# Optimization experiments

Measured on AMD Instinct MI355X. Metric: run time of the kernel, lower is better.

The kernel has to match this reference:

```python
import jax, jax.numpy as jnp
import numpy as np

B, H, S, D = 16, 12, 1024, 64  # batch, heads, seq, head_dim (dim=768, num_head=12)


def setup_inputs() -> dict:
    key = jax.random.key(0)
    ks = jax.random.split(key, 9)
    sc = 1.0 / np.sqrt(D)
    return {
        "x": jax.random.normal(ks[0], (B, H, S, D), dtype=jnp.float32),
        "Wq": jax.random.normal(ks[1], (D, D), dtype=jnp.float32) * sc,
        "bq": jax.random.normal(ks[2], (D,), dtype=jnp.float32) * 0.02,
        "Wk": jax.random.normal(ks[3], (D, D), dtype=jnp.float32) * sc,
        "bk": jax.random.normal(ks[4], (D,), dtype=jnp.float32) * 0.02,
        "Wv": jax.random.normal(ks[5], (D, D), dtype=jnp.float32) * sc,
        "bv": jax.random.normal(ks[6], (D,), dtype=jnp.float32) * 0.02,
        "Wo": jax.random.normal(ks[7], (D, D), dtype=jnp.float32) * sc,
        "bo": jax.random.normal(ks[8], (D,), dtype=jnp.float32) * 0.02,
    }


def reference(x, Wq, bq, Wk, bk, Wv, bv, Wo, bo):
    # torch Linear: y = x @ W^T + b, applied to last dim (head_dim)
    q = jnp.einsum("bhsd,ed->bhse", x, Wq) + bq
    k = jnp.einsum("bhsd,ed->bhse", x, Wk) + bk
    v = jnp.einsum("bhsd,ed->bhse", x, Wv) + bv
    scores = jnp.einsum("bhqd,bhkd->bhqk", q, k) / jnp.sqrt(jnp.float32(q.shape[-1]))
    attn = jax.nn.softmax(scores, axis=-1)
    out = jnp.einsum("bhqk,bhkd->bhqd", attn, v)
    out = jnp.einsum("bhsd,ed->bhse", out, Wo) + bo
    return out
```

## Files before the change

kernel.cpp:

```cpp
#include <hip/hip_runtime.h>
#include <math.h>


typedef __bf16 bf16x8 __attribute__((ext_vector_type(8)));
typedef float  f32x4  __attribute__((ext_vector_type(4)));

#define MFMA(a, b, c) __builtin_amdgcn_mfma_f32_16x16x32_bf16((a), (b), (c), 0, 0, 0)

static constexpr int S = 1024;
static constexpr int LDS_PAD = 72;
static constexpr size_t NE = 196608ull * 64ull;
static constexpr float QSCALE = 0.125f * 1.4426950408889634f;

__device__ inline unsigned long long pack4bf(float a, float b, float c, float d) {
    union { __bf16 h[4]; unsigned long long u; } pk;
    pk.h[0] = (__bf16)a; pk.h[1] = (__bf16)b; pk.h[2] = (__bf16)c; pk.h[3] = (__bf16)d;
    return pk.u;
}

__global__ __launch_bounds__(256) void proj_qkv(
    const float* __restrict__ x,
    const float* __restrict__ Wq, const float* __restrict__ bq,
    const float* __restrict__ Wk, const float* __restrict__ bk,
    const float* __restrict__ Wv, const float* __restrict__ bv,
    __bf16* __restrict__ gq, __bf16* __restrict__ gk, __bf16* __restrict__ gvt)
{
    __shared__ __align__(16) __bf16 lx[128][LDS_PAD];
    __shared__ __align__(16) __bf16 lw[3][64][LDS_PAD];
    __shared__ float lb[3][64];

    const int tid = threadIdx.x;
    const int row_base = blockIdx.x * 128;

    #pragma unroll
    for (int i = tid * 4; i < 8192; i += 1024) {
        float4 v = *(const float4*)(x + (size_t)row_base * 64 + i);
        int r = i >> 6, c = i & 63;
        *(unsigned long long*)&lx[r][c] = pack4bf(v.x, v.y, v.z, v.w);
    }
    const float* Ws[3] = {Wq, Wk, Wv};
    #pragma unroll
    for (int mtx = 0; mtx < 3; mtx++) {
        #pragma unroll
        for (int i = tid * 4; i < 4096; i += 1024) {
            float4 v = *(const float4*)(Ws[mtx] + i);
            int r = i >> 6, c = i & 63;
            *(unsigned long long*)&lw[mtx][r][c] = pack4bf(v.x, v.y, v.z, v.w);
        }
    }
    if (tid < 64) { lb[0][tid] = bq[tid]; lb[1][tid] = bk[tid]; lb[2][tid] = bv[tid]; }
    __syncthreads();

    const int w = tid >> 6, lane = tid & 63, m = lane & 15, quad = lane >> 4;
    const int bh = row_base >> 10;
    const int s_base = row_base & 1023;

    bf16x8 xf[2][2];
    #pragma unroll
    for (int g = 0; g < 2; g++) {
        xf[g][0] = *(const bf16x8*)&lx[w * 32 + g * 16 + m][quad * 8];
        xf[g][1] = *(const bf16x8*)&lx[w * 32 + g * 16 + m][32 + quad * 8];
    }

    #pragma unroll
    for (int mtx = 0; mtx < 3; mtx++) {
        #pragma unroll
        for (int et = 0; et < 4; et++) {
            bf16x8 wf0 = *(const bf16x8*)&lw[mtx][et * 16 + m][quad * 8];
            bf16x8 wf1 = *(const bf16x8*)&lw[mtx][et * 16 + m][32 + quad * 8];
            if (mtx < 2) {
                float4 bias = *(const float4*)&lb[mtx][et * 16 + quad * 4];
                #pragma unroll
                for (int g = 0; g < 2; g++) {
                    f32x4 acc = {0.f, 0.f, 0.f, 0.f};
                    acc = MFMA(wf0, xf[g][0], acc);
                    acc = MFMA(wf1, xf[g][1], acc);
                    size_t row = (size_t)row_base + w * 32 + g * 16 + m;
                    unsigned long long u;
                    if (mtx == 0)
                        u = pack4bf((acc[0] + bias.x) * QSCALE, (acc[1] + bias.y) * QSCALE,
                                    (acc[2] + bias.z) * QSCALE, (acc[3] + bias.w) * QSCALE);
                    else
                        u = pack4bf(acc[0] + bias.x, acc[1] + bias.y,
                                    acc[2] + bias.z, acc[3] + bias.w);
                    __bf16* dst = (mtx == 0 ? gq : gk);
                    *(unsigned long long*)(dst + row * 64 + et * 16 + quad * 4) = u;
                }
            } else {
                const int e = et * 16 + m;
                const float bias = lb[2][e];
                #pragma unroll
                for (int g = 0; g < 2; g++) {
                    f32x4 acc = {0.f, 0.f, 0.f, 0.f};
                    acc = MFMA(xf[g][0], wf0, acc);
                    acc = MFMA(xf[g][1], wf1, acc);
                    unsigned long long u = pack4bf(acc[0] + bias, acc[1] + bias,
                                                   acc[2] + bias, acc[3] + bias);
                    int sl = s_base + w * 32 + g * 16 + quad * 4;
                    *(unsigned long long*)(gvt + ((size_t)bh * 64 + e) * 1024 + sl) = u;
                }
            }
        }
    }
}

__global__ __launch_bounds__(256) void attn(
    const __bf16* __restrict__ gq, const __bf16* __restrict__ gk,
    const __bf16* __restrict__ gvt, __bf16* __restrict__ gao)
{
    __shared__ __align__(16) __bf16 lk[64][LDS_PAD];
    __shared__ __align__(16) __bf16 lv[80][LDS_PAD];
    __shared__ __align__(16) __bf16 lpT[4][32][LDS_PAD];

    const int tid = threadIdx.x;
    const int w = tid >> 6, lane = tid & 63, m = lane & 15, quad = lane >> 4;
    const int bh = blockIdx.x;
    const int q0 = blockIdx.y * 128 + w * 32;

    if (tid < 128) {
        uint4 ones;
        ones.x = 0x3F803F80u; ones.y = 0x3F803F80u;
        ones.z = 0x3F803F80u; ones.w = 0x3F803F80u;
        *(uint4*)&lv[64 + (tid >> 3)][(tid & 7) * 8] = ones;
    }

    bf16x8 qf[2][2];
    #pragma unroll
    for (int g = 0; g < 2; g++) {
        const __bf16* qrow = gq + ((size_t)bh * S + q0 + g * 16 + m) * 64;
        qf[g][0] = *(const bf16x8*)(qrow + quad * 8);
        qf[g][1] = *(const bf16x8*)(qrow + 32 + quad * 8);
    }

    f32x4 o[2][5];
    #pragma unroll
    for (int g = 0; g < 2; g++)
        #pragma unroll
        for (int n = 0; n < 5; n++) o[g][n] = {0.f, 0.f, 0.f, 0.f};

    const int sr = tid >> 3;
    const int sc = (tid & 7) * 8;
    const __bf16* kbase = gk + (size_t)bh * S * 64;
    const __bf16* vbase = gvt + (size_t)bh * 64 * 1024;

    uint4 kreg0 = *(const uint4*)(kbase + (size_t)sr * 64 + sc);
    uint4 kreg1 = *(const uint4*)(kbase + (size_t)(sr + 32) * 64 + sc);
    uint4 vreg0 = *(const uint4*)(vbase + (size_t)sr * 1024 + sc);
    uint4 vreg1 = *(const uint4*)(vbase + (size_t)(sr + 32) * 1024 + sc);

    for (int kb = 0; kb < 16; kb++) {
        __syncthreads();
        *(uint4*)&lk[sr][sc]      = kreg0;
        *(uint4*)&lk[sr + 32][sc] = kreg1;
        *(uint4*)&lv[sr][sc]      = vreg0;
        *(uint4*)&lv[sr + 32][sc] = vreg1;
        if (kb < 15) {
            const int nb = (kb + 1) * 64;
            kreg0 = *(const uint4*)(kbase + (size_t)(nb + sr) * 64 + sc);
            kreg1 = *(const uint4*)(kbase + (size_t)(nb + sr + 32) * 64 + sc);
            vreg0 = *(const uint4*)(vbase + (size_t)sr * 1024 + nb + sc);
            vreg1 = *(const uint4*)(vbase + (size_t)(sr + 32) * 1024 + nb + sc);
        }
        __syncthreads();

        #pragma unroll
        for (int t = 0; t < 4; t++) {
            bf16x8 ka0 = *(const bf16x8*)&lk[t * 16 + m][quad * 8];
            bf16x8 ka1 = *(const bf16x8*)&lk[t * 16 + m][32 + quad * 8];
            #pragma unroll
            for (int g = 0; g < 2; g++) {
                f32x4 acc = {0.f, 0.f, 0.f, 0.f};
                acc = MFMA(ka0, qf[g][0], acc);
                acc = MFMA(ka1, qf[g][1], acc);
                *(unsigned long long*)&lpT[w][g * 16 + m][t * 16 + quad * 4] =
                    pack4bf(__builtin_exp2f(acc[0]), __builtin_exp2f(acc[1]),
                            __builtin_exp2f(acc[2]), __builtin_exp2f(acc[3]));
            }
        }

        bf16x8 pb[2][2];
        #pragma unroll
        for (int g = 0; g < 2; g++) {
            pb[g][0] = *(const bf16x8*)&lpT[w][g * 16 + m][quad * 8];
            pb[g][1] = *(const bf16x8*)&lpT[w][g * 16 + m][32 + quad * 8];
        }
        #pragma unroll
        for (int n = 0; n < 5; n++) {
            bf16x8 va0 = *(const bf16x8*)&lv[n * 16 + m][quad * 8];
            bf16x8 va1 = *(const bf16x8*)&lv[n * 16 + m][32 + quad * 8];
            #pragma unroll
            for (int g = 0; g < 2; g++) {
                o[g][n] = MFMA(va0, pb[g][0], o[g][n]);
                o[g][n] = MFMA(va1, pb[g][1], o[g][n]);
            }
        }
    }

    #pragma unroll
    for (int g = 0; g < 2; g++) {
        const float inv = 1.f / o[g][4][0];
        __bf16* orow = gao + ((size_t)bh * S + q0 + g * 16 + m) * 64;
        #pragma unroll
        for (int n = 0; n < 4; n++) {
            *(unsigned long long*)(orow + n * 16 + quad * 4) =
                pack4bf(o[g][n][0] * inv, o[g][n][1] * inv,
                        o[g][n][2] * inv, o[g][n][3] * inv);
        }
    }
}

__global__ __launch_bounds__(256) void out_proj(
    const __bf16* __restrict__ gao, const float* __restrict__ Wo,
    const float* __restrict__ bo, float* __restrict__ out)
{
    __shared__ __align__(16) __bf16 lx[128][LDS_PAD];
    __shared__ __align__(16) __bf16 lw[64][LDS_PAD];
    __shared__ float lb[64];

    const int tid = threadIdx.x;
    const int row_base = blockIdx.x * 128;

    #pragma unroll
    for (int i = tid; i < 1024; i += 256) {
        int r = i >> 3, c = (i & 7) * 8;
        *(uint4*)&lx[r][c] = *(const uint4*)(gao + (size_t)row_base * 64 + r * 64 + c);
    }
    #pragma unroll
    for (int i = tid * 4; i < 4096; i += 1024) {
        float4 v = *(const float4*)(Wo + i);
        int r = i >> 6, c = i & 63;
        *(unsigned long long*)&lw[r][c] = pack4bf(v.x, v.y, v.z, v.w);
    }
    if (tid < 64) lb[tid] = bo[tid];
    __syncthreads();

    const int w = tid >> 6, lane = tid & 63, m = lane & 15, quad = lane >> 4;
    bf16x8 xf[2][2];
    #pragma unroll
    for (int g = 0; g < 2; g++) {
        xf[g][0] = *(const bf16x8*)&lx[w * 32 + g * 16 + m][quad * 8];
        xf[g][1] = *(const bf16x8*)&lx[w * 32 + g * 16 + m][32 + quad * 8];
    }

    #pragma unroll
    for (int et = 0; et < 4; et++) {
        bf16x8 wf0 = *(const bf16x8*)&lw[et * 16 + m][quad * 8];
        bf16x8 wf1 = *(const bf16x8*)&lw[et * 16 + m][32 + quad * 8];
        float4 bias = *(const float4*)&lb[et * 16 + quad * 4];
        #pragma unroll
        for (int g = 0; g < 2; g++) {
            f32x4 acc = {0.f, 0.f, 0.f, 0.f};
            acc = MFMA(wf0, xf[g][0], acc);
            acc = MFMA(wf1, xf[g][1], acc);
            float4 res;
            res.x = acc[0] + bias.x; res.y = acc[1] + bias.y;
            res.z = acc[2] + bias.z; res.w = acc[3] + bias.w;
            size_t row = (size_t)row_base + w * 32 + g * 16 + m;
            *(float4*)(out + row * 64 + et * 16 + quad * 4) = res;
        }
    }
}

extern "C" void kernel_launch(void* const* d_in, const int* in_sizes, int n_in,
                              void* d_out, int out_size, void* d_ws, size_t ws_size,
                              hipStream_t stream) {
    const float* x  = (const float*)d_in[0];
    const float* Wq = (const float*)d_in[1];
    const float* bq = (const float*)d_in[2];
    const float* Wk = (const float*)d_in[3];
    const float* bk = (const float*)d_in[4];
    const float* Wv = (const float*)d_in[5];
    const float* bv = (const float*)d_in[6];
    const float* Wo = (const float*)d_in[7];
    const float* bo = (const float*)d_in[8];
    float* out = (float*)d_out;

    __bf16* gq  = (__bf16*)d_ws;
    __bf16* gk  = gq + NE;
    __bf16* gvt = gk + NE;
    __bf16* gao = gvt + NE;

    proj_qkv<<<1536, 256, 0, stream>>>(x, Wq, bq, Wk, bk, Wv, bv, gq, gk, gvt);
    attn<<<dim3(192, 8), 256, 0, stream>>>(gq, gk, gvt, gao);
    out_proj<<<1536, 256, 0, stream>>>(gao, Wo, bo, out);
}
```

Baseline: 230.1 us.

## Fuse output projection into attention, double query tile, stage QKV stores via LDS

Folds the output projection into the attention kernel, so the bf16 attention output no longer round-trips through global memory and one launch goes away. Wo is converted to bf16 by a small pre-kernel. Each attention block now covers 256 queries (64 per wave) instead of 128, which halves K/V reloads per query. The row sum moves from an extra ones-row MFMA to register accumulation with shuffles. The QKV projection now stages its outputs through LDS so the global stores are coalesced 16-byte writes. The trade-offs are higher register pressure, fewer blocks (768) and scattered scalar fp32 output stores.

```diff
diff --git a/kernel.cpp b/kernel.cpp
--- a/kernel.cpp
+++ b/kernel.cpp
@@ -8,7 +8,7 @@
 #define MFMA(a, b, c) __builtin_amdgcn_mfma_f32_16x16x32_bf16((a), (b), (c), 0, 0, 0)
 
 static constexpr int S = 1024;
-static constexpr int LDS_PAD = 72;
+static constexpr int PAD = 72;
 static constexpr size_t NE = 196608ull * 64ull;
 static constexpr float QSCALE = 0.125f * 1.4426950408889634f;
 
@@ -16,6 +16,12 @@
     union { __bf16 h[4]; unsigned long long u; } pk;
     pk.h[0] = (__bf16)a; pk.h[1] = (__bf16)b; pk.h[2] = (__bf16)c; pk.h[3] = (__bf16)d;
     return pk.u;
+}
+
+__global__ void wo_conv(const float* __restrict__ Wo, __bf16* __restrict__ wob) {
+    int i = (blockIdx.x * 256 + threadIdx.x) * 4;
+    float4 v = *(const float4*)(Wo + i);
+    *(unsigned long long*)(wob + i) = pack4bf(v.x, v.y, v.z, v.w);
 }
 
 __global__ __launch_bounds__(256) void proj_qkv(
@@ -25,8 +31,9 @@
     const float* __restrict__ Wv, const float* __restrict__ bv,
     __bf16* __restrict__ gq, __bf16* __restrict__ gk, __bf16* __restrict__ gvt)
 {
-    __shared__ __align__(16) __bf16 lx[128][LDS_PAD];
-    __shared__ __align__(16) __bf16 lw[3][64][LDS_PAD];
+    __shared__ __align__(16) __bf16 lx[128][PAD];
+    __shared__ __align__(16) __bf16 lw[3][64][PAD];
+    __shared__ __align__(16) __bf16 lbuf[128][PAD];
     __shared__ float lb[3][64];
 
     const int tid = threadIdx.x;
@@ -63,80 +70,90 @@
     }
 
     #pragma unroll
-    for (int mtx = 0; mtx < 3; mtx++) {
+    for (int mtx = 0; mtx < 2; mtx++) {
         #pragma unroll
         for (int et = 0; et < 4; et++) {
             bf16x8 wf0 = *(const bf16x8*)&lw[mtx][et * 16 + m][quad * 8];
             bf16x8 wf1 = *(const bf16x8*)&lw[mtx][et * 16 + m][32 + quad * 8];
-            if (mtx < 2) {
-                float4 bias = *(const float4*)&lb[mtx][et * 16 + quad * 4];
-                #pragma unroll
-                for (int g = 0; g < 2; g++) {
-                    f32x4 acc = {0.f, 0.f, 0.f, 0.f};
-                    acc = MFMA(wf0, xf[g][0], acc);
-                    acc = MFMA(wf1, xf[g][1], acc);
-                    size_t row = (size_t)row_base + w * 32 + g * 16 + m;
-                    unsigned long long u;
-                    if (mtx == 0)
-                        u = pack4bf((acc[0] + bias.x) * QSCALE, (acc[1] + bias.y) * QSCALE,
-                                    (acc[2] + bias.z) * QSCALE, (acc[3] + bias.w) * QSCALE);
-                    else
-                        u = pack4bf(acc[0] + bias.x, acc[1] + bias.y,
-                                    acc[2] + bias.z, acc[3] + bias.w);
-                    __bf16* dst = (mtx == 0 ? gq : gk);
-                    *(unsigned long long*)(dst + row * 64 + et * 16 + quad * 4) = u;
-                }
-            } else {
-                const int e = et * 16 + m;
-                const float bias = lb[2][e];
-                #pragma unroll
-                for (int g = 0; g < 2; g++) {
-                    f32x4 acc = {0.f, 0.f, 0.f, 0.f};
-                    acc = MFMA(xf[g][0], wf0, acc);
-                    acc = MFMA(xf[g][1], wf1, acc);
-                    unsigned long long u = pack4bf(acc[0] + bias, acc[1] + bias,
-                                                   acc[2] + bias, acc[3] + bias);
-                    int sl = s_base + w * 32 + g * 16 + quad * 4;
-                    *(unsigned long long*)(gvt + ((size_t)bh * 64 + e) * 1024 + sl) = u;
-                }
-            }
-        }
+            float4 bias = *(const float4*)&lb[mtx][et * 16 + quad * 4];
+            #pragma unroll
+            for (int g = 0; g < 2; g++) {
+                f32x4 acc = {0.f, 0.f, 0.f, 0.f};
+                acc = MFMA(wf0, xf[g][0], acc);
+                acc = MFMA(wf1, xf[g][1], acc);
+                unsigned long long u;
+                if (mtx == 0)
+                    u = pack4bf((acc[0] + bias.x) * QSCALE, (acc[1] + bias.y) * QSCALE,
+                                (acc[2] + bias.z) * QSCALE, (acc[3] + bias.w) * QSCALE);
+                else
+                    u = pack4bf(acc[0] + bias.x, acc[1] + bias.y,
+                                acc[2] + bias.z, acc[3] + bias.w);
+                *(unsigned long long*)&lbuf[w * 32 + g * 16 + m][et * 16 + quad * 4] = u;
+            }
+        }
+        __syncthreads();
+        __bf16* dst = (mtx == 0 ? gq : gk);
+        #pragma unroll
+        for (int it = 0; it < 4; it++) {
+            int idx = it * 256 + tid;
+            int row = idx >> 3, col = (idx & 7) * 8;
+            *(uint4*)(dst + ((size_t)row_base + row) * 64 + col) = *(uint4*)&lbuf[row][col];
+        }
+        __syncthreads();
+    }
+
+    __bf16 (*lvt)[136] = (__bf16(*)[136])&lbuf[0][0];
+    #pragma unroll
+    for (int et = 0; et < 4; et++) {
+        bf16x8 wf0 = *(const bf16x8*)&lw[2][et * 16 + m][quad * 8];
+        bf16x8 wf1 = *(const bf16x8*)&lw[2][et * 16 + m][32 + quad * 8];
+        const float bias = lb[2][et * 16 + m];
+        #pragma unroll
+        for (int g = 0; g < 2; g++) {
+            f32x4 acc = {0.f, 0.f, 0.f, 0.f};
+            acc = MFMA(xf[g][0], wf0, acc);
+            acc = MFMA(xf[g][1], wf1, acc);
+            *(unsigned long long*)&lvt[et * 16 + m][w * 32 + g * 16 + quad * 4] =
+                pack4bf(acc[0] + bias, acc[1] + bias, acc[2] + bias, acc[3] + bias);
+        }
+    }
+    __syncthreads();
+    #pragma unroll
+    for (int it = 0; it < 4; it++) {
+        int idx = it * 256 + tid;
+        int row = idx >> 4, col = (idx & 15) * 8;
+        *(uint4*)(gvt + ((size_t)bh * 64 + row) * 1024 + s_base + col) = *(uint4*)&lvt[row][col];
     }
 }
 
 __global__ __launch_bounds__(256) void attn(
     const __bf16* __restrict__ gq, const __bf16* __restrict__ gk,
-    const __bf16* __restrict__ gvt, __bf16* __restrict__ gao)
+    const __bf16* __restrict__ gvt, const __bf16* __restrict__ wob,
+    const float* __restrict__ bo, float* __restrict__ out)
 {
-    __shared__ __align__(16) __bf16 lk[64][LDS_PAD];
-    __shared__ __align__(16) __bf16 lv[80][LDS_PAD];
-    __shared__ __align__(16) __bf16 lpT[4][32][LDS_PAD];
+    __shared__ __align__(16) __bf16 lk[64][PAD];
+    __shared__ __align__(16) __bf16 lv[64][PAD];
+    __shared__ __align__(16) __bf16 lp[4][64][PAD];
 
     const int tid = threadIdx.x;
     const int w = tid >> 6, lane = tid & 63, m = lane & 15, quad = lane >> 4;
     const int bh = blockIdx.x;
-    const int q0 = blockIdx.y * 128 + w * 32;
-
-    if (tid < 128) {
-        uint4 ones;
-        ones.x = 0x3F803F80u; ones.y = 0x3F803F80u;
-        ones.z = 0x3F803F80u; ones.w = 0x3F803F80u;
-        *(uint4*)&lv[64 + (tid >> 3)][(tid & 7) * 8] = ones;
-    }
-
-    bf16x8 qf[2][2];
-    #pragma unroll
-    for (int g = 0; g < 2; g++) {
+    const int q0 = blockIdx.y * 256 + w * 64;
+
+    bf16x8 qf[4][2];
+    #pragma unroll
+    for (int g = 0; g < 4; g++) {
         const __bf16* qrow = gq + ((size_t)bh * S + q0 + g * 16 + m) * 64;
         qf[g][0] = *(const bf16x8*)(qrow + quad * 8);
         qf[g][1] = *(const bf16x8*)(qrow + 32 + quad * 8);
     }
 
-    f32x4 o[2][5];
-    #pragma unroll
-    for (int g = 0; g < 2; g++)
-        #pragma unroll
-        for (int n = 0; n < 5; n++) o[g][n] = {0.f, 0.f, 0.f, 0.f};
+    f32x4 o[4][4];
+    float lsum[4] = {0.f, 0.f, 0.f, 0.f};
+    #pragma unroll
+    for (int g = 0; g < 4; g++)
+        #pragma unroll
+        for (int n = 0; n < 4; n++) o[g][n] = {0.f, 0.f, 0.f, 0.f};
 
     const int sr = tid >> 3;
     const int sc = (tid & 7) * 8;
@@ -168,28 +185,30 @@
             bf16x8 ka0 = *(const bf16x8*)&lk[t * 16 + m][quad * 8];
             bf16x8 ka1 = *(const bf16x8*)&lk[t * 16 + m][32 + quad * 8];
             #pragma unroll
-            for (int g = 0; g < 2; g++) {
+            for (int g = 0; g < 4; g++) {
                 f32x4 acc = {0.f, 0.f, 0.f, 0.f};
                 acc = MFMA(ka0, qf[g][0], acc);
                 acc = MFMA(ka1, qf[g][1], acc);
-                *(unsigned long long*)&lpT[w][g * 16 + m][t * 16 + quad * 4] =
-                    pack4bf(__builtin_exp2f(acc[0]), __builtin_exp2f(acc[1]),
-                            __builtin_exp2f(acc[2]), __builtin_exp2f(acc[3]));
-            }
-        }
-
-        bf16x8 pb[2][2];
-        #pragma unroll
-        for (int g = 0; g < 2; g++) {
-            pb[g][0] = *(const bf16x8*)&lpT[w][g * 16 + m][quad * 8];
-            pb[g][1] = *(const bf16x8*)&lpT[w][g * 16 + m][32 + quad * 8];
-        }
-        #pragma unroll
-        for (int n = 0; n < 5; n++) {
+                float e0 = __builtin_exp2f(acc[0]), e1 = __builtin_exp2f(acc[1]);
+                float e2 = __builtin_exp2f(acc[2]), e3 = __builtin_exp2f(acc[3]);
+                lsum[g] += (e0 + e1) + (e2 + e3);
+                *(unsigned long long*)&lp[w][g * 16 + m][t * 16 + quad * 4] =
+                    pack4bf(e0, e1, e2, e3);
+            }
+        }
+
+        bf16x8 pb[4][2];
+        #pragma unroll
+        for (int g = 0; g < 4; g++) {
+            pb[g][0] = *(const bf16x8*)&lp[w][g * 16 + m][quad * 8];
+            pb[g][1] = *(const bf16x8*)&lp[w][g * 16 + m][32 + quad * 8];
+        }
+        #pragma unroll
+        for (int n = 0; n < 4; n++) {
             bf16x8 va0 = *(const bf16x8*)&lv[n * 16 + m][quad * 8];
             bf16x8 va1 = *(const bf16x8*)&lv[n * 16 + m][32 + quad * 8];
             #pragma unroll
-            for (int g = 0; g < 2; g++) {
+            for (int g = 0; g < 4; g++) {
                 o[g][n] = MFMA(va0, pb[g][0], o[g][n]);
                 o[g][n] = MFMA(va1, pb[g][1], o[g][n]);
             }
@@ -197,66 +216,42 @@
     }
 
     #pragma unroll
-    for (int g = 0; g < 2; g++) {
-        const float inv = 1.f / o[g][4][0];
-        __bf16* orow = gao + ((size_t)bh * S + q0 + g * 16 + m) * 64;
+    for (int g = 0; g < 4; g++) {
+        lsum[g] += __shfl_xor(lsum[g], 16);
+        lsum[g] += __shfl_xor(lsum[g], 32);
+        const float inv = 1.f / lsum[g];
         #pragma unroll
         for (int n = 0; n < 4; n++) {
-            *(unsigned long long*)(orow + n * 16 + quad * 4) =
+            *(unsigned long long*)&lp[w][g * 16 + m][n * 16 + quad * 4] =
                 pack4bf(o[g][n][0] * inv, o[g][n][1] * inv,
                         o[g][n][2] * inv, o[g][n][3] * inv);
         }
     }
-}
-
-__global__ __launch_bounds__(256) void out_proj(
-    const __bf16* __restrict__ gao, const float* __restrict__ Wo,
-    const float* __restrict__ bo, float* __restrict__ out)
-{
-    __shared__ __align__(16) __bf16 lx[128][LDS_PAD];
-    __shared__ __align__(16) __bf16 lw[64][LDS_PAD];
-    __shared__ float lb[64];
-
-    const int tid = threadIdx.x;
-    const int row_base = blockIdx.x * 128;
-
-    #pragma unroll
-    for (int i = tid; i < 1024; i += 256) {
-        int r = i >> 3, c = (i & 7) * 8;
-        *(uint4*)&lx[r][c] = *(const uint4*)(gao + (size_t)row_base * 64 + r * 64 + c);
-    }
-    #pragma unroll
-    for (int i = tid * 4; i < 4096; i += 1024) {
-        float4 v = *(const float4*)(Wo + i);
-        int r = i >> 6, c = i & 63;
-        *(unsigned long long*)&lw[r][c] = pack4bf(v.x, v.y, v.z, v.w);
-    }
-    if (tid < 64) lb[tid] = bo[tid];
-    __syncthreads();
-
-    const int w = tid >> 6, lane = tid & 63, m = lane & 15, quad = lane >> 4;
-    bf16x8 xf[2][2];
-    #pragma unroll
-    for (int g = 0; g < 2; g++) {
-        xf[g][0] = *(const bf16x8*)&lx[w * 32 + g * 16 + m][quad * 8];
-        xf[g][1] = *(const bf16x8*)&lx[w * 32 + g * 16 + m][32 + quad * 8];
-    }
-
+
+    bf16x8 wf[4][2];
     #pragma unroll
     for (int et = 0; et < 4; et++) {
-        bf16x8 wf0 = *(const bf16x8*)&lw[et * 16 + m][quad * 8];
-        bf16x8 wf1 = *(const bf16x8*)&lw[et * 16 + m][32 + quad * 8];
-        float4 bias = *(const float4*)&lb[et * 16 + quad * 4];
-        #pragma unroll
-        for (int g = 0; g < 2; g++) {
+        wf[et][0] = *(const bf16x8*)(wob + (size_t)(et * 16 + m) * 64 + quad * 8);
+        wf[et][1] = *(const bf16x8*)(wob + (size_t)(et * 16 + m) * 64 + 32 + quad * 8);
+    }
+    float biasr[4];
+    #pragma unroll
+    for (int et = 0; et < 4; et++) biasr[et] = bo[et * 16 + m];
+
+    #pragma unroll
+    for (int g = 0; g < 4; g++) {
+        bf16x8 af0 = *(const bf16x8*)&lp[w][g * 16 + m][quad * 8];
+        bf16x8 af1 = *(const bf16x8*)&lp[w][g * 16 + m][32 + quad * 8];
+        #pragma unroll
+        for (int et = 0; et < 4; et++) {
             f32x4 acc = {0.f, 0.f, 0.f, 0.f};
-            acc = MFMA(wf0, xf[g][0], acc);
-            acc = MFMA(wf1, xf[g][1], acc);
-            float4 res;
-            res.x = acc[0] + bias.x; res.y = acc[1] + bias.y;
-            res.z = acc[2] + bias.z; res.w = acc[3] + bias.w;
-            size_t row = (size_t)row_base + w * 32 + g * 16 + m;
-            *(float4*)(out + row * 64 + et * 16 + quad * 4) = res;
+            acc = MFMA(af0, wf[et][0], acc);
+            acc = MFMA(af1, wf[et][1], acc);
+            #pragma unroll
+            for (int r = 0; r < 4; r++) {
+                size_t row = (size_t)bh * S + q0 + g * 16 + quad * 4 + r;
+                out[row * 64 + et * 16 + m] = acc[r] + biasr[et];
+            }
         }
     }
 }
@@ -278,9 +273,9 @@
     __bf16* gq  = (__bf16*)d_ws;
     __bf16* gk  = gq + NE;
     __bf16* gvt = gk + NE;
-    __bf16* gao = gvt + NE;
-
+    __bf16* wob = gvt + NE;
+
+    wo_conv<<<4, 256, 0, stream>>>(Wo, wob);
     proj_qkv<<<1536, 256, 0, stream>>>(x, Wq, bq, Wk, bk, Wv, bv, gq, gk, gvt);
-    attn<<<dim3(192, 8), 256, 0, stream>>>(gq, gk, gvt, gao);
-    out_proj<<<1536, 256, 0, stream>>>(gao, Wo, bo, out);
-}
+    attn<<<dim3(192, 4), 256, 0, stream>>>(gq, gk, gvt, wob, bo, out);
+}
```

Measured after the change: 227.5 us. No clear change (-1.1%).
